# Kernel optimization log

Hardware: AMD Instinct MI355X
Metric: run time of the kernel (lower is better)

## Reference

```python
import jax, jax.numpy as jnp
import numpy as np

OUT_CAPS_NUM = 16
OUT_CAPS_DIM = 512
ITER_NUM = 3
EPS = 1e-7


def setup_inputs() -> dict:
    key = jax.random.key(0)
    k_x, k_w = jax.random.split(key)
    x = jax.random.normal(k_x, (32, 128, 1024), dtype=jnp.float32)
    # xavier_normal-ish scale so tanh is not saturated
    W = jax.random.normal(k_w, (1024, OUT_CAPS_NUM * OUT_CAPS_DIM), dtype=jnp.float32) * 0.02
    return {"x": x, "W": W}


def _squash(S):
    # squash in source = divide by sqrt(||S||^2 + eps) (unit-ish norm)
    scale = jnp.sqrt(jnp.sum(S * S, axis=-1, keepdims=True) + EPS)
    return S / scale


def reference(x, W):
    b, s, _ = x.shape
    # caps_uhat: (b, s, out_caps_num, out_caps_dim)
    caps_uhat = jnp.tanh(jnp.einsum("bsd,dk->bsk", x, W)).reshape(
        b, s, OUT_CAPS_NUM, OUT_CAPS_DIM
    )
    B = jnp.zeros((b, s, OUT_CAPS_NUM), dtype=x.dtype)
    C_list = []
    B_logits = B
    V = None
    for _ in range(ITER_NUM):
        B_logits = B
        C = jax.nn.softmax(B, axis=2)          # (b, s, n)
        C_list.append(C)
        S = jnp.einsum("bsn,bsnd->bnd", C, caps_uhat)  # weighted sum over seq
        V = _squash(S)                          # (b, n, d)
        # agreement update: sum over caps dim
        B = jnp.einsum("bsnd,bnd->bsn", caps_uhat, V) + B
    C_ret = jnp.stack(C_list)                   # (iter, b, s, n)
    return (V, C_ret, B_logits)
```

## Files before the change

kernel.cpp:

```cpp
#include <hip/hip_runtime.h>
#include <math.h>

typedef float f32x4 __attribute__((ext_vector_type(4)));
typedef float f32x2 __attribute__((ext_vector_type(2)));
typedef int   i32x4 __attribute__((ext_vector_type(4)));
typedef unsigned short u16;
typedef u16 u16x4 __attribute__((ext_vector_type(4)));

#define NG 8192
#define KG 1024

__device__ __forceinline__ u16 f2bf(float f) {
  unsigned u = __builtin_bit_cast(unsigned, f);
  u += 0x7fffu + ((u >> 16) & 1u);
  return (u16)(u >> 16);
}
__device__ __forceinline__ float bflo(unsigned u) {
  return __builtin_bit_cast(float, u << 16);
}
__device__ __forceinline__ float bfhi(unsigned u) {
  return __builtin_bit_cast(float, u & 0xffff0000u);
}

__device__ __forceinline__ void gload16(const void* g, void* l) {
  __builtin_amdgcn_global_load_lds(
      (const __attribute__((address_space(1))) void*)g,
      (__attribute__((address_space(3))) void*)l, 16, 0, 0);
}

__device__ __forceinline__ f32x4 mfma_bf16(i32x4 a, i32x4 b, f32x4 c) {
  asm("v_mfma_f32_16x16x32_bf16 %0, %1, %2, %0" : "+v"(c) : "v"(a), "v"(b));
  return c;
}

__device__ __forceinline__ float fast_tanh(float x) {
  float ax = fabsf(x);
  float e = __expf(-2.0f * ax);
  float r = (1.0f - e) * __frcp_rn(1.0f + e);
  return copysignf(r, x);
}

__global__ __launch_bounds__(256) void k_convx(const float* __restrict__ x,
                                               u16* __restrict__ xb) {
  int i = blockIdx.x * 256 + threadIdx.x;
  f32x4 v = ((const f32x4*)x)[i];
  u16x4 r = { f2bf(v.x), f2bf(v.y), f2bf(v.z), f2bf(v.w) };
  ((u16x4*)xb)[i] = r;
}

__global__ __launch_bounds__(256) void k_transW(const float* __restrict__ W,
                                                u16* __restrict__ wt) {
  __shared__ float tile[32][33];
  const int n0 = blockIdx.x * 32;
  const int k0 = blockIdx.y * 32;
  const int tx = threadIdx.x & 31;
  const int ty = threadIdx.x >> 5;
#pragma unroll
  for (int r = 0; r < 32; r += 8)
    tile[ty + r][tx] = W[(size_t)(k0 + ty + r) * NG + n0 + tx];
  __syncthreads();
#pragma unroll
  for (int r = 0; r < 32; r += 8)
    wt[(size_t)(n0 + ty + r) * KG + k0 + tx] = f2bf(tile[tx][ty + r]);
}

__global__ __launch_bounds__(256) void k_init(float* __restrict__ C0,
                                              float* __restrict__ Bws) {
  int i = blockIdx.x * 256 + threadIdx.x;
  f32x4 c = { 0.0625f, 0.0625f, 0.0625f, 0.0625f };
  f32x4 z = {};
  ((f32x4*)C0)[i] = c;
  ((f32x4*)Bws)[i] = z;
}

__global__ __launch_bounds__(256) void k_gemm_tanh(const u16* __restrict__ xb,
                                                   const u16* __restrict__ wt,
                                                   u16* __restrict__ uhat) {
  __shared__ u16 As[2][128 * 32];
  __shared__ u16 Bs[2][128 * 32];
  const int m0 = blockIdx.y * 128;
  const int n0 = blockIdx.x * 128;
  const int t = threadIdx.x;
  const int lane = t & 63;
  const int wave = t >> 6;
  const int wr = (wave >> 1) * 64;
  const int wc = (wave & 1) * 64;
  f32x4 acc[4][4] = {};

  const int r0 = t >> 2;
  const int r1 = 64 + (t >> 2);
  const int c0 = (t & 3) * 8;
  const u16* ga0 = xb + (size_t)(m0 + r0) * KG + c0;
  const u16* ga1 = xb + (size_t)(m0 + r1) * KG + c0;
  const u16* gb0 = wt + (size_t)(n0 + r0) * KG + c0;
  const u16* gb1 = wt + (size_t)(n0 + r1) * KG + c0;

  const int am = lane & 15;
  const int ak = (lane >> 4) * 8;

  for (int kt = 0; kt < KG; kt += 64) {
#pragma unroll
    for (int kh = 0; kh < 2; ++kh) {
      const int ko = kt + kh * 32;
      gload16(ga0 + ko, &As[kh][t * 8]);
      gload16(ga1 + ko, &As[kh][(256 + t) * 8]);
      gload16(gb0 + ko, &Bs[kh][t * 8]);
      gload16(gb1 + ko, &Bs[kh][(256 + t) * 8]);
    }
    __syncthreads();
#pragma unroll
    for (int kh = 0; kh < 2; ++kh) {
      i32x4 af[4], bf[4];
#pragma unroll
      for (int mi = 0; mi < 4; ++mi)
        af[mi] = *(const i32x4*)&As[kh][(wr + mi * 16 + am) * 32 + ak];
#pragma unroll
      for (int ni = 0; ni < 4; ++ni)
        bf[ni] = *(const i32x4*)&Bs[kh][(wc + ni * 16 + am) * 32 + ak];
#pragma unroll
      for (int mi = 0; mi < 4; ++mi)
#pragma unroll
        for (int ni = 0; ni < 4; ++ni)
          acc[mi][ni] = mfma_bf16(af[mi], bf[ni], acc[mi][ni]);
    }
    __syncthreads();
  }

  const int crow0 = (lane >> 4) * 4;
  const int ccol = lane & 15;
#pragma unroll
  for (int mi = 0; mi < 4; ++mi)
#pragma unroll
    for (int ni = 0; ni < 4; ++ni)
#pragma unroll
      for (int j = 0; j < 4; ++j) {
        int row = m0 + wr + mi * 16 + crow0 + j;
        int col = n0 + wc + ni * 16 + ccol;
        uhat[(size_t)row * NG + col] = f2bf(fast_tanh(acc[mi][ni][j]));
      }
}

__global__ __launch_bounds__(256) void k_spass(const u16* __restrict__ uhat,
                                               const float* __restrict__ C,
                                               float* __restrict__ V) {
  const int n = blockIdx.x;
  const int b = blockIdx.y;
  const int t = threadIdx.x;
  const int g = t >> 6;
  const int dl = t & 63;
  __shared__ float cl[128];
  __shared__ float Sred[4][512];
  if (t < 128) cl[t] = C[((size_t)b * 128 + t) * 16 + n];
  __syncthreads();

  const u16* up = uhat + (((size_t)b * 128) * 16 + n) * 512 + dl * 8;
  float a[8] = {};
#pragma unroll 4
  for (int i = 0; i < 32; ++i) {
    const int s = g + i * 4;
    i32x4 u = *(const i32x4*)(up + (size_t)s * NG);
    float c = cl[s];
    a[0] = fmaf(c, bflo(u.x), a[0]); a[1] = fmaf(c, bfhi(u.x), a[1]);
    a[2] = fmaf(c, bflo(u.y), a[2]); a[3] = fmaf(c, bfhi(u.y), a[3]);
    a[4] = fmaf(c, bflo(u.z), a[4]); a[5] = fmaf(c, bfhi(u.z), a[5]);
    a[6] = fmaf(c, bflo(u.w), a[6]); a[7] = fmaf(c, bfhi(u.w), a[7]);
  }
#pragma unroll
  for (int e = 0; e < 8; ++e) Sred[g][dl * 8 + e] = a[e];
  __syncthreads();

  if (g == 0) {
    float S[8];
    float ss = 0.f;
#pragma unroll
    for (int e = 0; e < 8; ++e) {
      int d = dl * 8 + e;
      S[e] = Sred[0][d] + Sred[1][d] + Sred[2][d] + Sred[3][d];
      ss = fmaf(S[e], S[e], ss);
    }
#pragma unroll
    for (int m = 1; m < 64; m <<= 1) ss += __shfl_xor(ss, m);
    float r = rsqrtf(ss + 1e-7f);
    float* vp = V + ((size_t)b * 16 + n) * 512 + dl * 8;
    f32x4 v0 = { S[0] * r, S[1] * r, S[2] * r, S[3] * r };
    f32x4 v1 = { S[4] * r, S[5] * r, S[6] * r, S[7] * r };
    *(f32x4*)vp = v0;
    *(f32x4*)(vp + 4) = v1;
  }
}

__global__ __launch_bounds__(256) void k_bupdate(const u16* __restrict__ uhat,
                                                 const float* __restrict__ V,
                                                 float* __restrict__ Bws,
                                                 float* __restrict__ Cnext,
                                                 float* __restrict__ Blog) {
  const int bs = blockIdx.x;
  const int b = bs >> 7;
  const int t = threadIdx.x;
  const int n = t >> 4;
  const int j = t & 15;
  const u16* up = uhat + ((size_t)bs * 16 + n) * 512 + j * 32;
  const float* vp = V + ((size_t)b * 16 + n) * 512 + j * 32;
  float dot = 0.f;
#pragma unroll
  for (int q = 0; q < 4; ++q) {
    i32x4 u = *(const i32x4*)(up + q * 8);
    f32x4 v0 = *(const f32x4*)(vp + q * 8);
    f32x4 v1 = *(const f32x4*)(vp + q * 8 + 4);
    dot = fmaf(bflo(u.x), v0.x, dot);
    dot = fmaf(bfhi(u.x), v0.y, dot);
    dot = fmaf(bflo(u.y), v0.z, dot);
    dot = fmaf(bfhi(u.y), v0.w, dot);
    dot = fmaf(bflo(u.z), v1.x, dot);
    dot = fmaf(bfhi(u.z), v1.y, dot);
    dot = fmaf(bflo(u.w), v1.z, dot);
    dot = fmaf(bfhi(u.w), v1.w, dot);
  }
#pragma unroll
  for (int m = 1; m < 16; m <<= 1) dot += __shfl_xor(dot, m);
  __shared__ float bl[16];
  if (j == 0) bl[n] = Bws[(size_t)bs * 16 + n] + dot;
  __syncthreads();
  if (t < 16) {
    float mx = -1e30f;
#pragma unroll
    for (int k2 = 0; k2 < 16; ++k2) mx = fmaxf(mx, bl[k2]);
    float e = expf(bl[t] - mx);
    float sum = 0.f;
#pragma unroll
    for (int k2 = 0; k2 < 16; ++k2) sum += expf(bl[k2] - mx);
    size_t o = (size_t)bs * 16 + t;
    Cnext[o] = e / sum;
    float bn = bl[t];
    Bws[o] = bn;
    if (Blog) Blog[o] = bn;
  }
}

extern "C" void kernel_launch(void* const* d_in, const int* in_sizes, int n_in,
                              void* d_out, int out_size, void* d_ws, size_t ws_size,
                              hipStream_t stream) {
  const float* x = (const float*)d_in[0];
  const float* W = (const float*)d_in[1];
  float* out = (float*)d_out;
  float* Vout = out;
  float* Cout = out + 262144;
  float* Blog = out + 262144 + 196608;

  char* ws = (char*)d_ws;
  u16* uhat = (u16*)ws;
  u16* xb   = (u16*)(ws + 67108864);
  u16* wt   = (u16*)(ws + 67108864 + 8388608);
  float* Vws = (float*)(ws + 92274688);
  float* Bws = (float*)(ws + 93323264);

  k_convx<<<4096, 256, 0, stream>>>(x, xb);
  k_transW<<<dim3(256, 32), 256, 0, stream>>>(W, wt);
  k_init<<<64, 256, 0, stream>>>(Cout, Bws);
  k_gemm_tanh<<<dim3(64, 32), 256, 0, stream>>>(xb, wt, uhat);
  k_spass<<<dim3(16, 32), 256, 0, stream>>>(uhat, Cout, Vws);
  k_bupdate<<<4096, 256, 0, stream>>>(uhat, Vws, Bws, Cout + 65536, nullptr);
  k_spass<<<dim3(16, 32), 256, 0, stream>>>(uhat, Cout + 65536, Vws);
  k_bupdate<<<4096, 256, 0, stream>>>(uhat, Vws, Bws, Cout + 2 * 65536, Blog);
  k_spass<<<dim3(16, 32), 256, 0, stream>>>(uhat, Cout + 2 * 65536, Vout);
}
```

Before: 272.9 us.

## Fuse S-pass and B-update via LDS-resident uhat tile per (b,n) block

Each block now loads its 128x512 bf16 uhat slice into shared memory with an XOR swizzle. It computes S and V from that copy, then reuses the same LDS data for the agreement dot product, writing per-(s,n) dots. A small softmax kernel handles the B accumulation and the C update. This removes the second full read of the 64MB uhat on each iteration. The cost is 128KB of LDS per block, which limits occupancy to one block per CU with only 512 blocks in the grid.

```diff
diff --git a/kernel.cpp b/kernel.cpp
--- a/kernel.cpp
+++ b/kernel.cpp
@@ -2,7 +2,6 @@
 #include <math.h>
 
 typedef float f32x4 __attribute__((ext_vector_type(4)));
-typedef float f32x2 __attribute__((ext_vector_type(2)));
 typedef int   i32x4 __attribute__((ext_vector_type(4)));
 typedef unsigned short u16;
 typedef u16 u16x4 __attribute__((ext_vector_type(4)));
@@ -140,25 +139,35 @@
       }
 }
 
-__global__ __launch_bounds__(256) void k_spass(const u16* __restrict__ uhat,
+template <int MODE>
+__global__ __launch_bounds__(256) void k_fused(const u16* __restrict__ uhat,
                                                const float* __restrict__ C,
-                                               float* __restrict__ V) {
+                                               float* __restrict__ dst) {
+  __shared__ u16 Us[128 * 512];
+  __shared__ float cl[128];
+  __shared__ float Sred[4][512];
   const int n = blockIdx.x;
   const int b = blockIdx.y;
   const int t = threadIdx.x;
-  const int g = t >> 6;
-  const int dl = t & 63;
-  __shared__ float cl[128];
-  __shared__ float Sred[4][512];
+  const int lane = t & 63;
+  const int wave = t >> 6;
+  const u16* Ub = uhat + ((size_t)b * 128) * NG + n * 512;
+
   if (t < 128) cl[t] = C[((size_t)b * 128 + t) * 16 + n];
+
+#pragma unroll 8
+  for (int i = 0; i < 32; ++i) {
+    const int row = i * 4 + wave;
+    gload16(Ub + (size_t)row * NG + ((lane ^ (row & 7)) * 8),
+            &Us[row * 512 + lane * 8]);
+  }
   __syncthreads();
 
-  const u16* up = uhat + (((size_t)b * 128) * 16 + n) * 512 + dl * 8;
   float a[8] = {};
-#pragma unroll 4
+#pragma unroll 8
   for (int i = 0; i < 32; ++i) {
-    const int s = g + i * 4;
-    i32x4 u = *(const i32x4*)(up + (size_t)s * NG);
+    const int s = wave + i * 4;
+    i32x4 u = *(const i32x4*)&Us[s * 512 + ((lane ^ (s & 7)) * 8)];
     float c = cl[s];
     a[0] = fmaf(c, bflo(u.x), a[0]); a[1] = fmaf(c, bfhi(u.x), a[1]);
     a[2] = fmaf(c, bflo(u.y), a[2]); a[3] = fmaf(c, bfhi(u.y), a[3]);
@@ -166,74 +175,93 @@
     a[6] = fmaf(c, bflo(u.w), a[6]); a[7] = fmaf(c, bfhi(u.w), a[7]);
   }
 #pragma unroll
-  for (int e = 0; e < 8; ++e) Sred[g][dl * 8 + e] = a[e];
+  for (int e = 0; e < 8; ++e) Sred[wave][lane * 8 + e] = a[e];
   __syncthreads();
 
-  if (g == 0) {
+  if (wave == 0) {
     float S[8];
     float ss = 0.f;
 #pragma unroll
     for (int e = 0; e < 8; ++e) {
-      int d = dl * 8 + e;
+      int d = lane * 8 + e;
       S[e] = Sred[0][d] + Sred[1][d] + Sred[2][d] + Sred[3][d];
       ss = fmaf(S[e], S[e], ss);
     }
 #pragma unroll
     for (int m = 1; m < 64; m <<= 1) ss += __shfl_xor(ss, m);
     float r = rsqrtf(ss + 1e-7f);
-    float* vp = V + ((size_t)b * 16 + n) * 512 + dl * 8;
-    f32x4 v0 = { S[0] * r, S[1] * r, S[2] * r, S[3] * r };
-    f32x4 v1 = { S[4] * r, S[5] * r, S[6] * r, S[7] * r };
-    *(f32x4*)vp = v0;
-    *(f32x4*)(vp + 4) = v1;
-  }
-}
-
-__global__ __launch_bounds__(256) void k_bupdate(const u16* __restrict__ uhat,
-                                                 const float* __restrict__ V,
-                                                 float* __restrict__ Bws,
-                                                 float* __restrict__ Cnext,
-                                                 float* __restrict__ Blog) {
-  const int bs = blockIdx.x;
-  const int b = bs >> 7;
-  const int t = threadIdx.x;
-  const int n = t >> 4;
-  const int j = t & 15;
-  const u16* up = uhat + ((size_t)bs * 16 + n) * 512 + j * 32;
-  const float* vp = V + ((size_t)b * 16 + n) * 512 + j * 32;
-  float dot = 0.f;
+    if (MODE == 1) {
+      float* vp = dst + ((size_t)b * 16 + n) * 512 + lane * 8;
+      f32x4 v0 = { S[0] * r, S[1] * r, S[2] * r, S[3] * r };
+      f32x4 v1 = { S[4] * r, S[5] * r, S[6] * r, S[7] * r };
+      *(f32x4*)vp = v0;
+      *(f32x4*)(vp + 4) = v1;
+    } else {
+#pragma unroll
+      for (int e = 0; e < 8; ++e) Sred[0][lane * 8 + e] = S[e] * r;
+    }
+  }
+
+  if (MODE == 0) {
+    __syncthreads();
+    const int s = t >> 1, h = t & 1;
+    const float* Vl = &Sred[0][0];
+    float dot = 0.f;
+#pragma unroll 8
+    for (int i = 0; i < 32; ++i) {
+      const int chunk = h * 32 + i;
+      i32x4 u = *(const i32x4*)&Us[s * 512 + ((chunk ^ (s & 7)) * 8)];
+      const float* vp = Vl + chunk * 8;
+      f32x4 v0 = *(const f32x4*)vp;
+      f32x4 v1 = *(const f32x4*)(vp + 4);
+      dot = fmaf(bflo(u.x), v0.x, dot);
+      dot = fmaf(bfhi(u.x), v0.y, dot);
+      dot = fmaf(bflo(u.y), v0.z, dot);
+      dot = fmaf(bfhi(u.y), v0.w, dot);
+      dot = fmaf(bflo(u.z), v1.x, dot);
+      dot = fmaf(bfhi(u.z), v1.y, dot);
+      dot = fmaf(bflo(u.w), v1.z, dot);
+      dot = fmaf(bfhi(u.w), v1.w, dot);
+    }
+    dot += __shfl_xor(dot, 1);
+    if (h == 0) dst[((size_t)b * 128 + s) * 16 + n] = dot;
+  }
+}
+
+__global__ __launch_bounds__(256) void k_bsm(const float* __restrict__ dotB,
+                                             float* __restrict__ Bws,
+                                             float* __restrict__ Cnext,
+                                             float* __restrict__ Blog) {
+  int row = blockIdx.x * 256 + threadIdx.x;
+  size_t o = (size_t)row * 16;
+  f32x4 bv[4];
 #pragma unroll
   for (int q = 0; q < 4; ++q) {
-    i32x4 u = *(const i32x4*)(up + q * 8);
-    f32x4 v0 = *(const f32x4*)(vp + q * 8);
-    f32x4 v1 = *(const f32x4*)(vp + q * 8 + 4);
-    dot = fmaf(bflo(u.x), v0.x, dot);
-    dot = fmaf(bfhi(u.x), v0.y, dot);
-    dot = fmaf(bflo(u.y), v0.z, dot);
-    dot = fmaf(bfhi(u.y), v0.w, dot);
-    dot = fmaf(bflo(u.z), v1.x, dot);
-    dot = fmaf(bfhi(u.z), v1.y, dot);
-    dot = fmaf(bflo(u.w), v1.z, dot);
-    dot = fmaf(bfhi(u.w), v1.w, dot);
-  }
-#pragma unroll
-  for (int m = 1; m < 16; m <<= 1) dot += __shfl_xor(dot, m);
-  __shared__ float bl[16];
-  if (j == 0) bl[n] = Bws[(size_t)bs * 16 + n] + dot;
-  __syncthreads();
-  if (t < 16) {
-    float mx = -1e30f;
-#pragma unroll
-    for (int k2 = 0; k2 < 16; ++k2) mx = fmaxf(mx, bl[k2]);
-    float e = expf(bl[t] - mx);
-    float sum = 0.f;
-#pragma unroll
-    for (int k2 = 0; k2 < 16; ++k2) sum += expf(bl[k2] - mx);
-    size_t o = (size_t)bs * 16 + t;
-    Cnext[o] = e / sum;
-    float bn = bl[t];
-    Bws[o] = bn;
-    if (Blog) Blog[o] = bn;
+    f32x4 p = *(const f32x4*)(Bws + o + q * 4);
+    f32x4 d = *(const f32x4*)(dotB + o + q * 4);
+    bv[q].x = p.x + d.x; bv[q].y = p.y + d.y;
+    bv[q].z = p.z + d.z; bv[q].w = p.w + d.w;
+  }
+  float mx = -1e30f;
+#pragma unroll
+  for (int q = 0; q < 4; ++q)
+    mx = fmaxf(mx, fmaxf(fmaxf(bv[q].x, bv[q].y), fmaxf(bv[q].z, bv[q].w)));
+  f32x4 ev[4];
+  float sum = 0.f;
+#pragma unroll
+  for (int q = 0; q < 4; ++q) {
+    ev[q].x = __expf(bv[q].x - mx); sum += ev[q].x;
+    ev[q].y = __expf(bv[q].y - mx); sum += ev[q].y;
+    ev[q].z = __expf(bv[q].z - mx); sum += ev[q].z;
+    ev[q].w = __expf(bv[q].w - mx); sum += ev[q].w;
+  }
+  float r = __frcp_rn(sum);
+#pragma unroll
+  for (int q = 0; q < 4; ++q) {
+    ev[q].x *= r; ev[q].y *= r; ev[q].z *= r; ev[q].w *= r;
+    *(f32x4*)(Cnext + o + q * 4) = ev[q];
+    *(f32x4*)(Bws + o + q * 4) = bv[q];
+    if (Blog) *(f32x4*)(Blog + o + q * 4) = bv[q];
   }
 }
 
@@ -250,17 +278,17 @@
   char* ws = (char*)d_ws;
   u16* uhat = (u16*)ws;
   u16* xb   = (u16*)(ws + 67108864);
-  u16* wt   = (u16*)(ws + 67108864 + 8388608);
-  float* Vws = (float*)(ws + 92274688);
-  float* Bws = (float*)(ws + 93323264);
+  u16* wt   = (u16*)(ws + 75497472);
+  float* dotB = (float*)(ws + 92274688);
+  float* Bws  = (float*)(ws + 92536832);
 
   k_convx<<<4096, 256, 0, stream>>>(x, xb);
   k_transW<<<dim3(256, 32), 256, 0, stream>>>(W, wt);
   k_init<<<64, 256, 0, stream>>>(Cout, Bws);
   k_gemm_tanh<<<dim3(64, 32), 256, 0, stream>>>(xb, wt, uhat);
-  k_spass<<<dim3(16, 32), 256, 0, stream>>>(uhat, Cout, Vws);
-  k_bupdate<<<4096, 256, 0, stream>>>(uhat, Vws, Bws, Cout + 65536, nullptr);
-  k_spass<<<dim3(16, 32), 256, 0, stream>>>(uhat, Cout + 65536, Vws);
-  k_bupdate<<<4096, 256, 0, stream>>>(uhat, Vws, Bws, Cout + 2 * 65536, Blog);
-  k_spass<<<dim3(16, 32), 256, 0, stream>>>(uhat, Cout + 2 * 65536, Vout);
-}
+  k_fused<0><<<dim3(16, 32), 256, 0, stream>>>(uhat, Cout, dotB);
+  k_bsm<<<16, 256, 0, stream>>>(dotB, Bws, Cout + 65536, nullptr);
+  k_fused<0><<<dim3(16, 32), 256, 0, stream>>>(uhat, Cout + 65536, dotB);
+  k_bsm<<<16, 256, 0, stream>>>(dotB, Bws, Cout + 2 * 65536, Blog);
+  k_fused<1><<<dim3(16, 32), 256, 0, stream>>>(uhat, Cout + 2 * 65536, Vout);
+}
```

Measured after the change: 237.3 us. -13.0%, faster.
